# Optimization experiments

Hardware: AMD Instinct MI355X
Metric: run time of the kernel (lower is better)

Reference implementation:

```python
import jax, jax.numpy as jnp
import numpy as np


def setup_inputs() -> dict:
    key = jax.random.key(0)
    k1, k2, k3 = jax.random.split(key, 3)
    B, C_IN, C_OUT, R, K = 4, 64, 64, 64, 3
    x = jax.random.normal(k1, (B, C_IN, R, R, R), dtype=jnp.float32)
    # per-voxel nonzero test |x|.sum(channel) != 0 used by the module)
    keep = jax.random.uniform(k2, (B, 1, R, R, R)) < 0.3
    x = x * keep.astype(jnp.float32)
    weight = jax.random.normal(k3, (C_OUT, C_IN, K, K, K), dtype=jnp.float32)
    return {"x": x, "weight": weight}


def reference(x, weight):
    # The torch module gathers a k^3 neighborhood at every nonzero input voxel,
    # contracts with the (unflipped) weight, and scatters to the same voxel.
    # This is exactly cross-correlation (torch conv semantics) with SAME padding,
    # masked to voxels where the input is nonzero across channels.
    K = weight.shape[-1]
    pad_l = K // 2
    pad_r = K - 1 - pad_l
    out = jax.lax.conv_general_dilated(
        x, weight,
        window_strides=(1, 1, 1),
        padding=[(pad_l, pad_r)] * 3,
        dimension_numbers=("NCDHW", "OIDHW", "NCDHW"),
    )  # [B, C_out, D, H, W]
    mask = (jnp.abs(x).sum(axis=1, keepdims=True) != 0)  # [B,1,D,H,W]
    return out * mask.astype(out.dtype)
```

## Files before the change

### kernel.cpp

```cpp
#include <hip/hip_runtime.h>
#include <stdint.h>


#define R3 262144
#define NVOX (4 * R3)
#define WSW_ELEMS (27 * 2 * 4 * 64 * 8)

typedef __attribute__((ext_vector_type(4))) float f32x4;
typedef __attribute__((ext_vector_type(8))) short short8;

static __device__ inline unsigned short f2bf(float f) {
    union { float f; unsigned u; } v; v.f = f;
    unsigned u = v.u;
    return (unsigned short)((u + 0x7fffu + ((u >> 16) & 1u)) >> 16);
}

__global__ void wprep(const float* __restrict__ w, unsigned short* __restrict__ wsw) {
    int e = blockIdx.x * 256 + threadIdx.x;
    if (e >= WSW_ELEMS) return;
    int j    = e & 7;
    int lane = (e >> 3) & 63;
    int nt   = (e >> 9) & 3;
    int kc   = (e >> 11) & 1;
    int tap  = e >> 12;
    int co = nt * 16 + (lane & 15);
    int ci = kc * 32 + ((lane >> 4) * 8) + j;
    wsw[e] = f2bf(w[(co * 64 + ci) * 27 + tap]);
}

__global__ void __launch_bounds__(256) xprep(const float* __restrict__ x,
                                             unsigned int* __restrict__ xt_u32,
                                             int* __restrict__ list,
                                             int* __restrict__ count) {
    __shared__ unsigned int lds[256 * 33];
    __shared__ unsigned int wcnt[4], wbase[4], bbase;
    int t = threadIdx.x;
    int v = blockIdx.x * 256 + t;
    int b = v >> 18;
    int s = v & (R3 - 1);
    const float* xb = x + (size_t)b * (64 * R3) + s;
    bool active = false;
#pragma unroll
    for (int c2 = 0; c2 < 32; ++c2) {
        float f0 = xb[(size_t)(2 * c2) * R3];
        float f1 = xb[(size_t)(2 * c2 + 1) * R3];
        active |= (f0 != 0.f) | (f1 != 0.f);
        lds[t * 33 + c2] = (unsigned)f2bf(f0) | ((unsigned)f2bf(f1) << 16);
    }
    __syncthreads();
    unsigned int* dst = xt_u32 + (size_t)blockIdx.x * 8192;
#pragma unroll
    for (int i = 0; i < 32; ++i) {
        int g = i * 256 + t;
        dst[g] = lds[(g >> 5) * 33 + (g & 31)];
    }
    int lane = t & 63, w = t >> 6;
    unsigned long long bal = __ballot(active);
    if (lane == 0) wcnt[w] = (unsigned)__popcll(bal);
    __syncthreads();
    if (t == 0) {
        unsigned tot = 0;
        for (int i = 0; i < 4; ++i) { wbase[i] = tot; tot += wcnt[i]; }
        bbase = (unsigned)atomicAdd(count, (int)tot);
    }
    __syncthreads();
    if (active) {
        unsigned pos = bbase + wbase[w] + (unsigned)__popcll(bal & ((1ULL << lane) - 1ULL));
        list[pos] = v;
    }
}

__global__ void __launch_bounds__(256) sconv_gemm(const unsigned short* __restrict__ xt,
                                                  const unsigned short* __restrict__ wsw,
                                                  const int* __restrict__ list,
                                                  const int* __restrict__ count_p,
                                                  float* __restrict__ out) {
    __shared__ __align__(16) unsigned short Alds[64 * 72];
    __shared__ int vids[64];
    int count = *count_p;
    int base = blockIdx.x * 64;
    if (base >= count) return;
    int t = threadIdx.x;
    if (t < 64) {
        int idx = base + t;
        vids[t] = (idx < count) ? list[idx] : -1;
    }
    __syncthreads();

    int lane = t & 63, w = t >> 6;
    int mt0 = (w & 1) * 2, nt0 = (w >> 1) * 2;
    f32x4 acc[2][2] = {};

    int srow = t >> 2;
    int scol = t & 3;
    int vid = vids[srow];
    bool vvalid = vid >= 0;
    int vx = vid & 63, vy = (vid >> 6) & 63, vz = (vid >> 12) & 63;
    int vbase = vid & ~(R3 - 1);

    for (int tap = 0; tap < 27; ++tap) {
        int dz = tap / 9 - 1, dy = (tap / 3) % 3 - 1, dx = tap % 3 - 1;
        uint4 val0 = {0, 0, 0, 0}, val1 = {0, 0, 0, 0};
        if (vvalid) {
            int nz = vz + dz, ny = vy + dy, nx = vx + dx;
            if ((unsigned)nz < 64u && (unsigned)ny < 64u && (unsigned)nx < 64u) {
                long long ns = (long long)vbase + nz * 4096 + ny * 64 + nx;
                const uint4* src = (const uint4*)(xt + (size_t)ns * 64) + scol * 2;
                val0 = src[0];
                val1 = src[1];
            }
        }
        *(uint4*)&Alds[srow * 72 + scol * 16] = val0;
        *(uint4*)&Alds[srow * 72 + scol * 16 + 8] = val1;
        __syncthreads();

#pragma unroll
        for (int kc = 0; kc < 2; ++kc) {
            short8 bfr[2], afr[2];
#pragma unroll
            for (int n = 0; n < 2; ++n) {
                int nt = nt0 + n;
                bfr[n] = *(const short8*)(wsw +
                          (((size_t)(tap * 8 + kc * 4 + nt)) * 64 + lane) * 8);
            }
#pragma unroll
            for (int m = 0; m < 2; ++m) {
                int row = (mt0 + m) * 16 + (lane & 15);
                afr[m] = *(const short8*)&Alds[row * 72 + kc * 32 + (lane >> 4) * 8];
            }
#pragma unroll
            for (int m = 0; m < 2; ++m)
#pragma unroll
                for (int n = 0; n < 2; ++n)
                    acc[m][n] = __builtin_amdgcn_mfma_f32_16x16x32_bf16(
                        afr[m], bfr[n], acc[m][n], 0, 0, 0);
        }
        __syncthreads();
    }

    int q = lane >> 4;
#pragma unroll
    for (int m = 0; m < 2; ++m) {
#pragma unroll
        for (int rg = 0; rg < 4; ++rg) {
            int row = (mt0 + m) * 16 + q * 4 + rg;
            if (base + row < count) {
                int vv = vids[row];
                int bb = vv >> 18;
                int sp = vv & (R3 - 1);
#pragma unroll
                for (int n = 0; n < 2; ++n) {
                    int co = (nt0 + n) * 16 + (lane & 15);
                    out[((size_t)(bb * 64 + co)) * R3 + sp] = acc[m][n][rg];
                }
            }
        }
    }
}

__global__ void __launch_bounds__(64) fallback_conv(const float* __restrict__ x,
                                                    const float* __restrict__ wt,
                                                    float* __restrict__ out) {
    __shared__ float rowb[66];
    int bid = blockIdx.x;
    int y = bid & 63, z = (bid >> 6) & 63, co = (bid >> 12) & 63, b = bid >> 18;
    int t = threadIdx.x;
    float acc = 0.f;
    bool active = false;
    for (int ci = 0; ci < 64; ++ci) {
        const float* xp = x + ((size_t)(b * 64 + ci)) * R3;
        const float* wp = wt + ((size_t)(co * 64 + ci)) * 27;
        for (int dz = -1; dz <= 1; ++dz) {
            int nz = z + dz;
            bool okz = (unsigned)nz < 64u;
            for (int dy = -1; dy <= 1; ++dy) {
                int ny = y + dy;
                bool ok = okz && ((unsigned)ny < 64u);
                float v = ok ? xp[nz * 4096 + ny * 64 + t] : 0.f;
                rowb[t + 1] = v;
                if (t == 0) { rowb[0] = 0.f; rowb[65] = 0.f; }
                __syncthreads();
                if (dz == 0 && dy == 0) active |= (rowb[t + 1] != 0.f);
                const float* wq = wp + (dz + 1) * 9 + (dy + 1) * 3;
                acc += rowb[t] * wq[0] + rowb[t + 1] * wq[1] + rowb[t + 2] * wq[2];
                __syncthreads();
            }
        }
    }
    out[((size_t)(b * 64 + co)) * R3 + z * 4096 + y * 64 + t] = active ? acc : 0.f;
}

extern "C" void kernel_launch(void* const* d_in, const int* in_sizes, int n_in,
                              void* d_out, int out_size, void* d_ws, size_t ws_size,
                              hipStream_t stream) {
    const float* x = (const float*)d_in[0];
    const float* w = (const float*)d_in[1];
    float* out = (float*)d_out;

    const size_t XT_BYTES  = (size_t)NVOX * 64 * 2;
    const size_t LIST_OFF  = XT_BYTES;
    const size_t WSW_OFF   = LIST_OFF + (size_t)NVOX * 4;
    const size_t CNT_OFF   = WSW_OFF + (size_t)WSW_ELEMS * 2;
    const size_t NEED      = CNT_OFF + 256;

    if (ws_size < NEED) {
        fallback_conv<<<NVOX, 64, 0, stream>>>(x, w, out);
        return;
    }

    unsigned int*   xt   = (unsigned int*)d_ws;
    int*            list = (int*)((char*)d_ws + LIST_OFF);
    unsigned short* wsw  = (unsigned short*)((char*)d_ws + WSW_OFF);
    int*            cnt  = (int*)((char*)d_ws + CNT_OFF);

    hipMemsetAsync(cnt, 0, sizeof(int), stream);
    hipMemsetAsync(d_out, 0, (size_t)out_size * sizeof(float), stream);
    wprep<<<WSW_ELEMS / 256, 256, 0, stream>>>(w, wsw);
    xprep<<<NVOX / 256, 256, 0, stream>>>(x, xt, list, cnt);
    sconv_gemm<<<NVOX / 64, 256, 0, stream>>>((const unsigned short*)xt, wsw, list, cnt, out);
}
```

Baseline: 710.8 us.

## Replace sparse gather GEMM with dense row-based implicit-GEMM conv plus bitmask epilogue

Replaces the compacted active-voxel list and per-voxel neighbour gather with a dense implicit GEMM. Each one-wave block handles a full 64-voxel x-row and stages the 9 (dz,dy) neighbour rows in LDS, reusing each row across the three dx taps. The next row is prefetched into registers while the current one is used. The output is masked with a per-voxel bitmask and written through an LDS transpose for coalesced stores, which removes the atomic list build and the full-output memset. In exchange it does dense compute on inactive voxels, about 3.3x more MFMA work at 30% density.

```diff
diff --git a/kernel.cpp b/kernel.cpp
--- a/kernel.cpp
+++ b/kernel.cpp
@@ -30,10 +30,8 @@
 
 __global__ void __launch_bounds__(256) xprep(const float* __restrict__ x,
                                              unsigned int* __restrict__ xt_u32,
-                                             int* __restrict__ list,
-                                             int* __restrict__ count) {
+                                             unsigned int* __restrict__ maskbits) {
     __shared__ unsigned int lds[256 * 33];
-    __shared__ unsigned int wcnt[4], wbase[4], bbase;
     int t = threadIdx.x;
     int v = blockIdx.x * 256 + t;
     int b = v >> 18;
@@ -54,106 +52,109 @@
         int g = i * 256 + t;
         dst[g] = lds[(g >> 5) * 33 + (g & 31)];
     }
-    int lane = t & 63, w = t >> 6;
     unsigned long long bal = __ballot(active);
-    if (lane == 0) wcnt[w] = (unsigned)__popcll(bal);
-    __syncthreads();
-    if (t == 0) {
-        unsigned tot = 0;
-        for (int i = 0; i < 4; ++i) { wbase[i] = tot; tot += wcnt[i]; }
-        bbase = (unsigned)atomicAdd(count, (int)tot);
-    }
-    __syncthreads();
-    if (active) {
-        unsigned pos = bbase + wbase[w] + (unsigned)__popcll(bal & ((1ULL << lane) - 1ULL));
-        list[pos] = v;
-    }
-}
-
-__global__ void __launch_bounds__(256) sconv_gemm(const unsigned short* __restrict__ xt,
-                                                  const unsigned short* __restrict__ wsw,
-                                                  const int* __restrict__ list,
-                                                  const int* __restrict__ count_p,
-                                                  float* __restrict__ out) {
-    __shared__ __align__(16) unsigned short Alds[64 * 72];
-    __shared__ int vids[64];
-    int count = *count_p;
-    int base = blockIdx.x * 64;
-    if (base >= count) return;
-    int t = threadIdx.x;
-    if (t < 64) {
-        int idx = base + t;
-        vids[t] = (idx < count) ? list[idx] : -1;
-    }
-    __syncthreads();
-
-    int lane = t & 63, w = t >> 6;
-    int mt0 = (w & 1) * 2, nt0 = (w >> 1) * 2;
-    f32x4 acc[2][2] = {};
-
-    int srow = t >> 2;
-    int scol = t & 3;
-    int vid = vids[srow];
-    bool vvalid = vid >= 0;
-    int vx = vid & 63, vy = (vid >> 6) & 63, vz = (vid >> 12) & 63;
-    int vbase = vid & ~(R3 - 1);
-
-    for (int tap = 0; tap < 27; ++tap) {
-        int dz = tap / 9 - 1, dy = (tap / 3) % 3 - 1, dx = tap % 3 - 1;
-        uint4 val0 = {0, 0, 0, 0}, val1 = {0, 0, 0, 0};
-        if (vvalid) {
-            int nz = vz + dz, ny = vy + dy, nx = vx + dx;
-            if ((unsigned)nz < 64u && (unsigned)ny < 64u && (unsigned)nx < 64u) {
-                long long ns = (long long)vbase + nz * 4096 + ny * 64 + nx;
-                const uint4* src = (const uint4*)(xt + (size_t)ns * 64) + scol * 2;
-                val0 = src[0];
-                val1 = src[1];
-            }
-        }
-        *(uint4*)&Alds[srow * 72 + scol * 16] = val0;
-        *(uint4*)&Alds[srow * 72 + scol * 16 + 8] = val1;
-        __syncthreads();
-
-#pragma unroll
-        for (int kc = 0; kc < 2; ++kc) {
-            short8 bfr[2], afr[2];
-#pragma unroll
-            for (int n = 0; n < 2; ++n) {
-                int nt = nt0 + n;
-                bfr[n] = *(const short8*)(wsw +
-                          (((size_t)(tap * 8 + kc * 4 + nt)) * 64 + lane) * 8);
-            }
-#pragma unroll
-            for (int m = 0; m < 2; ++m) {
-                int row = (mt0 + m) * 16 + (lane & 15);
-                afr[m] = *(const short8*)&Alds[row * 72 + kc * 32 + (lane >> 4) * 8];
-            }
-#pragma unroll
-            for (int m = 0; m < 2; ++m)
-#pragma unroll
-                for (int n = 0; n < 2; ++n)
-                    acc[m][n] = __builtin_amdgcn_mfma_f32_16x16x32_bf16(
-                        afr[m], bfr[n], acc[m][n], 0, 0, 0);
-        }
-        __syncthreads();
-    }
-
-    int q = lane >> 4;
-#pragma unroll
-    for (int m = 0; m < 2; ++m) {
-#pragma unroll
-        for (int rg = 0; rg < 4; ++rg) {
-            int row = (mt0 + m) * 16 + q * 4 + rg;
-            if (base + row < count) {
-                int vv = vids[row];
-                int bb = vv >> 18;
-                int sp = vv & (R3 - 1);
-#pragma unroll
-                for (int n = 0; n < 2; ++n) {
-                    int co = (nt0 + n) * 16 + (lane & 15);
-                    out[((size_t)(bb * 64 + co)) * R3 + sp] = acc[m][n][rg];
+    if ((t & 63) == 0) {
+        unsigned base = ((unsigned)blockIdx.x * 256 + (t >> 6) * 64) >> 5;
+        maskbits[base]     = (unsigned)bal;
+        maskbits[base + 1] = (unsigned)(bal >> 32);
+    }
+}
+
+__global__ void __launch_bounds__(64, 3) sconv_dense(const unsigned short* __restrict__ xt,
+                                                     const unsigned short* __restrict__ wsw,
+                                                     const unsigned int* __restrict__ maskbits,
+                                                     float* __restrict__ out) {
+    __shared__ __align__(16) unsigned short smem[66 * 72];
+    int bid = blockIdx.x;
+    int lin = (bid & 7) * 2048 + (bid >> 3);
+    int b = lin >> 12, z = (lin >> 6) & 63, y = lin & 63;
+    int l = threadIdx.x, q = l >> 4, lm = l & 15;
+
+    unsigned int* sw = (unsigned int*)smem;
+    if (l < 32) sw[l] = 0u;
+    else        sw[65 * 36 + (l - 32)] = 0u;
+
+    f32x4 acc[4][4] = {};
+    uint4 rg[8];
+
+    bool vcur;
+    {
+        int zp = z + 0 - 1, yp = y + 0 - 1;
+        vcur = ((unsigned)zp < 64u) & ((unsigned)yp < 64u);
+        if (vcur) {
+            const uint4* g = (const uint4*)(xt + ((size_t)b * R3 + zp * 4096 + yp * 64) * 64);
+#pragma unroll
+            for (int k = 0; k < 8; ++k) rg[k] = g[k * 64 + l];
+        }
+    }
+
+    for (int s = 0; s < 9; ++s) {
+        if (vcur) {
+#pragma unroll
+            for (int k = 0; k < 8; ++k) {
+                int c = k * 64 + l;
+                int row = (c >> 3) + 1;
+                *(uint4*)&smem[row * 72 + (c & 7) * 8] = rg[k];
+            }
+        }
+        bool vnext = false;
+        if (s < 8) {
+            int sn = s + 1;
+            int zp = z + sn / 3 - 1, yp = y + sn % 3 - 1;
+            vnext = ((unsigned)zp < 64u) & ((unsigned)yp < 64u);
+            if (vnext) {
+                const uint4* g = (const uint4*)(xt + ((size_t)b * R3 + zp * 4096 + yp * 64) * 64);
+#pragma unroll
+                for (int k = 0; k < 8; ++k) rg[k] = g[k * 64 + l];
+            }
+        }
+        if (vcur) {
+            int tapb = (s / 3) * 9 + (s % 3) * 3;
+#pragma unroll
+            for (int dx = 0; dx < 3; ++dx) {
+#pragma unroll
+                for (int kc = 0; kc < 2; ++kc) {
+                    short8 afr[4], bfr[4];
+#pragma unroll
+                    for (int nt = 0; nt < 4; ++nt)
+                        bfr[nt] = *(const short8*)(wsw +
+                            (((size_t)((tapb + dx) * 8 + kc * 4 + nt)) * 64 + l) * 8);
+#pragma unroll
+                    for (int mt = 0; mt < 4; ++mt) {
+                        int row = mt * 16 + lm + dx;
+                        afr[mt] = *(const short8*)&smem[row * 72 + kc * 32 + q * 8];
+                    }
+#pragma unroll
+                    for (int mt = 0; mt < 4; ++mt)
+#pragma unroll
+                        for (int nt = 0; nt < 4; ++nt)
+                            acc[mt][nt] = __builtin_amdgcn_mfma_f32_16x16x32_bf16(
+                                afr[mt], bfr[nt], acc[mt][nt], 0, 0, 0);
                 }
             }
+        }
+        vcur = vnext;
+    }
+
+    long long v0 = (long long)b * R3 + z * 4096 + y * 64;
+    unsigned mw0 = maskbits[(v0 >> 5)];
+    unsigned mw1 = maskbits[(v0 >> 5) + 1];
+    float* epi = (float*)smem;
+#pragma unroll
+    for (int mt = 0; mt < 4; ++mt) {
+#pragma unroll
+        for (int nt = 0; nt < 4; ++nt)
+#pragma unroll
+            for (int r = 0; r < 4; ++r)
+                epi[(nt * 16 + lm) * 17 + q * 4 + r] = acc[mt][nt][r];
+        unsigned mw = (mt < 2) ? mw0 : mw1;
+#pragma unroll
+        for (int rr = 0; rr < 16; ++rr) {
+            int co = rr * 4 + q;
+            float val = epi[co * 17 + lm];
+            int xg = mt * 16 + lm;
+            val = ((mw >> (xg & 31)) & 1u) ? val : 0.0f;
+            out[(size_t)(b * 64 + co) * R3 + z * 4096 + y * 64 + xg] = val;
         }
     }
 }
@@ -197,25 +198,21 @@
     const float* w = (const float*)d_in[1];
     float* out = (float*)d_out;
 
-    const size_t XT_BYTES  = (size_t)NVOX * 64 * 2;
-    const size_t LIST_OFF  = XT_BYTES;
-    const size_t WSW_OFF   = LIST_OFF + (size_t)NVOX * 4;
-    const size_t CNT_OFF   = WSW_OFF + (size_t)WSW_ELEMS * 2;
-    const size_t NEED      = CNT_OFF + 256;
+    const size_t XT_BYTES = (size_t)NVOX * 64 * 2;
+    const size_t MB_OFF   = XT_BYTES;
+    const size_t WSW_OFF  = MB_OFF + NVOX / 8;
+    const size_t NEED     = WSW_OFF + (size_t)WSW_ELEMS * 2;
 
     if (ws_size < NEED) {
         fallback_conv<<<NVOX, 64, 0, stream>>>(x, w, out);
         return;
     }
 
-    unsigned int*   xt   = (unsigned int*)d_ws;
-    int*            list = (int*)((char*)d_ws + LIST_OFF);
-    unsigned short* wsw  = (unsigned short*)((char*)d_ws + WSW_OFF);
-    int*            cnt  = (int*)((char*)d_ws + CNT_OFF);
-
-    hipMemsetAsync(cnt, 0, sizeof(int), stream);
-    hipMemsetAsync(d_out, 0, (size_t)out_size * sizeof(float), stream);
+    unsigned int*   xt_u32 = (unsigned int*)d_ws;
+    unsigned int*   mbits  = (unsigned int*)((char*)d_ws + MB_OFF);
+    unsigned short* wsw    = (unsigned short*)((char*)d_ws + WSW_OFF);
+
     wprep<<<WSW_ELEMS / 256, 256, 0, stream>>>(w, wsw);
-    xprep<<<NVOX / 256, 256, 0, stream>>>(x, xt, list, cnt);
-    sconv_gemm<<<NVOX / 64, 256, 0, stream>>>((const unsigned short*)xt, wsw, list, cnt, out);
-}
+    xprep<<<NVOX / 256, 256, 0, stream>>>(x, xt_u32, mbits);
+    sconv_dense<<<NVOX / 64, 64, 0, stream>>>((const unsigned short*)xt_u32, wsw, mbits, out);
+}
```

New measurement: 1.009 ms. 42.0% more time.
